# Optimization experiments

Hardware: AMD Instinct MI355X
Metric: run time of the kernel (lower is better)

The kernel has to match this reference:

```python
import jax, jax.numpy as jnp
import numpy as np
import math

QK_DIM = 128

def setup_inputs() -> dict:
    key = jax.random.key(0)
    kx, kq, kk, kv = jax.random.split(key, 4)
    B, S, D, H = 4, 4096, 1024, 128
    X = jax.random.normal(kx, (B, S, D), dtype=jnp.float32)
    # xavier-normal-ish scale for weights
    std = math.sqrt(2.0 / (D + H))
    W_q = jax.random.normal(kq, (D, H), dtype=jnp.float32) * std
    W_k = jax.random.normal(kk, (D, H), dtype=jnp.float32) * std
    W_v = jax.random.normal(kv, (D, H), dtype=jnp.float32) * std
    return {"X": X, "W_q": W_q, "W_k": W_k, "W_v": W_v}

def reference(X, W_q, W_k, W_v):
    # X: [B, S, D]; single-head causal attention
    Q = X @ W_q                       # [B, S, H]
    K = X @ W_k                       # [B, S, H]
    V = X @ W_v                       # [B, S, H]
    S_len = X.shape[1]
    scores = jnp.einsum('bsh,bth->bst', Q, K) / math.sqrt(QK_DIM)  # [B, S, S]
    causal = jnp.tril(jnp.ones((S_len, S_len), dtype=bool))
    scores = jnp.where(causal, scores, -jnp.inf)
    attn = jax.nn.softmax(scores, axis=-1)
    return jnp.einsum('bst,bth->bsh', attn, V)
```

## Files before the change

### kernel.cpp

```cpp
#include <hip/hip_runtime.h>
#include <hip/hip_bf16.h>

#define B_ 4
#define S_ 4096
#define D_ 1024
#define H_ 128

typedef unsigned short u16;
typedef unsigned int u32;
typedef short s16x8 __attribute__((ext_vector_type(8)));
typedef float f32x4 __attribute__((ext_vector_type(4)));
typedef float f32x16 __attribute__((ext_vector_type(16)));

__device__ __forceinline__ u16 f2bf(float f) {
    u32 x = __float_as_uint(f);
    u32 r = x + 0x7fffu + ((x >> 16) & 1u);
    return (u16)(r >> 16);
}

__device__ __forceinline__ u32 cvtpk_bf16(float a, float b) {
    u32 r;
    asm("v_cvt_pk_bf16_f32 %0, %1, %2" : "=v"(r) : "v"(a), "v"(b));
    return r;
}
__device__ __forceinline__ void pl32swap(u32& x, u32& y) {
    asm("v_permlane32_swap_b32 %0, %1" : "+v"(x), "+v"(y));
}

__device__ __forceinline__ void gl_lds16(const u16* g, u16* l) {
    __builtin_amdgcn_global_load_lds(
        (const __attribute__((address_space(1))) u32*)g,
        (__attribute__((address_space(3))) u32*)l, 16, 0, 0);
}

__global__ void detect_dtype_kernel(const u32* __restrict__ w, int* __restrict__ flag) {
    __shared__ int smax[256];
    const int tid = threadIdx.x;
    int m = 0;
    for (int i = tid; i < 1024; i += 256) {
        u32 x = w[i];
        m = max(m, max((int)((x >> 7) & 0xFF), (int)((x >> 23) & 0xFF)));
    }
    smax[tid] = m;
    __syncthreads();
    if (tid == 0) {
        int mm = 0;
        for (int i = 0; i < 256; ++i) mm = max(mm, smax[i]);
        *flag = (mm >= 200) ? 1 : 0;
    }
}

__global__ __launch_bounds__(256) void prep_w_kernel(
    const void* __restrict__ Wq, const void* __restrict__ Wk, const void* __restrict__ Wv,
    u16* __restrict__ Wt, const int* __restrict__ dflag)
{
    const int kt = blockIdx.x, mat = blockIdx.y;
    const void* W = (mat == 0) ? Wq : (mat == 1) ? Wk : Wv;
    const int isf = *dflag;
    const int t = threadIdx.x;
    const int kk = t >> 3;
    const int n0 = (t & 7) * 16;
    u16 vals[16];
    if (isf) {
        const float* wp = (const float*)W + (size_t)(kt * 32 + kk) * H_ + n0;
#pragma unroll
        for (int i = 0; i < 16; ++i) vals[i] = f2bf(wp[i]);
    } else {
        const u16* wp = (const u16*)W + (size_t)(kt * 32 + kk) * H_ + n0;
#pragma unroll
        for (int i = 0; i < 16; ++i) vals[i] = wp[i];
    }
    const size_t base = (size_t)(mat * 32 + kt) * 128;
#pragma unroll
    for (int i = 0; i < 16; ++i)
        Wt[(base + n0 + i) * 32 + kk] = vals[i];
}

__global__ __launch_bounds__(256) void qkv_kernel(
    const void* __restrict__ Xv, const u16* __restrict__ Wt,
    u16* __restrict__ Qo, u16* __restrict__ Ko, u16* __restrict__ Vto,
    const int* __restrict__ dflag)
{
    __shared__ u16 Ws[2][384 * 32];
    __shared__ union { u16 qk[32 * 136]; u16 vt[128 * 40]; } OsU;

    const int isf = *dflag;
    const int tid = threadIdx.x;
    const int w = tid >> 6, lane = tid & 63;
    const int r = lane & 15, q = lane >> 4;
    const size_t m0 = (size_t)blockIdx.x * 32;

    f32x4 acc[2][6];
#pragma unroll
    for (int s2 = 0; s2 < 2; ++s2)
#pragma unroll
        for (int i = 0; i < 6; ++i) acc[s2][i] = (f32x4){0.f, 0.f, 0.f, 0.f};

    const float* xf0 = (const float*)Xv + (m0 + r) * D_;
    const float* xf1 = (const float*)Xv + (m0 + 16 + r) * D_;
    const u16*   xb0 = (const u16*)Xv + (m0 + r) * D_;
    const u16*   xb1 = (const u16*)Xv + (m0 + 16 + r) * D_;

    float4 af[2][2];
    uint4  ab[2];

#pragma unroll
    for (int i = 0; i < 6; ++i) {
        int c = tid + i * 256;
        gl_lds16(Wt + (size_t)((c >> 9) * 32) * 4096 + (c & 511) * 8, &Ws[0][c * 8]);
    }
    if (isf) {
        af[0][0] = *(const float4*)(xf0 + q * 8);
        af[0][1] = *(const float4*)(xf0 + q * 8 + 4);
        af[1][0] = *(const float4*)(xf1 + q * 8);
        af[1][1] = *(const float4*)(xf1 + q * 8 + 4);
    } else {
        ab[0] = *(const uint4*)(xb0 + q * 8);
        ab[1] = *(const uint4*)(xb1 + q * 8);
    }

    for (int kt = 0; kt < 32; ++kt) {
        const int buf = kt & 1;
        __syncthreads();

        if (kt + 1 < 32) {
#pragma unroll
            for (int i = 0; i < 6; ++i) {
                int c = tid + i * 256;
                gl_lds16(Wt + (size_t)((c >> 9) * 32 + kt + 1) * 4096 + (c & 511) * 8,
                         &Ws[buf ^ 1][c * 8]);
            }
        }

        s16x8 a[2];
        if (isf) {
#pragma unroll
            for (int s2 = 0; s2 < 2; ++s2) {
                union { u16 u[8]; s16x8 v; } pk;
                pk.u[0] = f2bf(af[s2][0].x); pk.u[1] = f2bf(af[s2][0].y);
                pk.u[2] = f2bf(af[s2][0].z); pk.u[3] = f2bf(af[s2][0].w);
                pk.u[4] = f2bf(af[s2][1].x); pk.u[5] = f2bf(af[s2][1].y);
                pk.u[6] = f2bf(af[s2][1].z); pk.u[7] = f2bf(af[s2][1].w);
                a[s2] = pk.v;
            }
        } else {
            a[0] = *(const s16x8*)&ab[0];
            a[1] = *(const s16x8*)&ab[1];
        }

        if (kt + 1 < 32) {
            const int k0 = (kt + 1) * 32;
            if (isf) {
                af[0][0] = *(const float4*)(xf0 + k0 + q * 8);
                af[0][1] = *(const float4*)(xf0 + k0 + q * 8 + 4);
                af[1][0] = *(const float4*)(xf1 + k0 + q * 8);
                af[1][1] = *(const float4*)(xf1 + k0 + q * 8 + 4);
            } else {
                ab[0] = *(const uint4*)(xb0 + k0 + q * 8);
                ab[1] = *(const uint4*)(xb1 + k0 + q * 8);
            }
        }

#pragma unroll
        for (int i = 0; i < 6; ++i) {
            int c = w * 6 + i;
            s16x8 b = *(const s16x8*)&Ws[buf][(c >> 3) * 4096 + ((c & 7) * 16 + r) * 32 + q * 8];
            acc[0][i] = __builtin_amdgcn_mfma_f32_16x16x32_bf16(a[0], b, acc[0][i], 0, 0, 0);
            acc[1][i] = __builtin_amdgcn_mfma_f32_16x16x32_bf16(a[1], b, acc[1][i], 0, 0, 0);
        }
    }

    u16* outs[2] = {Qo, Ko};
    for (int m = 0; m < 2; ++m) {
        const float sc = (m == 0) ? 0.08838834764831845f : 1.0f;
        __syncthreads();
#pragma unroll
        for (int i = 0; i < 6; ++i) {
            int c = w * 6 + i;
            if ((c >> 3) == m) {
                int nt = c & 7;
#pragma unroll
                for (int s2 = 0; s2 < 2; ++s2)
#pragma unroll
                    for (int reg = 0; reg < 4; ++reg)
                        OsU.qk[(s2 * 16 + q * 4 + reg) * 136 + nt * 16 + r] = f2bf(acc[s2][i][reg] * sc);
            }
        }
        __syncthreads();
        u16* Out = outs[m];
#pragma unroll
        for (int it = 0; it < 2; ++it) {
            int c = tid + it * 256;
            int row = c >> 4, col = (c & 15) * 8;
            *(uint4*)(Out + (m0 + row) * H_ + col) = *(const uint4*)&OsU.qk[row * 136 + col];
        }
    }

    __syncthreads();
#pragma unroll
    for (int i = 0; i < 6; ++i) {
        int c = w * 6 + i;
        if ((c >> 3) == 2) {
            int nt = c & 7;
#pragma unroll
            for (int s2 = 0; s2 < 2; ++s2)
#pragma unroll
                for (int reg = 0; reg < 4; ++reg)
                    OsU.vt[(nt * 16 + r) * 40 + s2 * 16 + q * 4 + reg] = f2bf(acc[s2][i][reg]);
        }
    }
    __syncthreads();
    {
        const int bb = blockIdx.x >> 7;
        const int s0 = (blockIdx.x & 127) * 32;
#pragma unroll
        for (int it = 0; it < 2; ++it) {
            int c = tid + it * 256;
            int h = c >> 2, sh = (c & 3) * 8;
            *(uint4*)(Vto + ((size_t)bb * H_ + h) * S_ + s0 + sh) =
                *(const uint4*)&OsU.vt[h * 40 + sh];
        }
    }
}

__global__ __launch_bounds__(512) void attn_pair_kernel(
    const u16* __restrict__ Q, const u16* __restrict__ K, const u16* __restrict__ Vt,
    void* __restrict__ out, float* __restrict__ OP, float* __restrict__ LP,
    const int* __restrict__ dflag)
{
    __shared__ u16 Ks[2][128 * 128];
    __shared__ u16 Vs[2][128 * 128];
    __shared__ float lpS[8][32];

    const int isf = *dflag;
    const int tid = threadIdx.x;
    const int w = tid >> 6, lane = tid & 63;
    const int l31 = lane & 31, hi = lane >> 5;
    const int qs = w >> 2;
    const int kh = w & 3;
    const int bid = blockIdx.x;
    const int b = bid & 3;
    const int p = (bid >> 2) & 31;
    const int c = bid >> 7;
    const int nA = (p >> 1) + 1;
    const int m = 17 - nA;

    const u16* Kg  = K  + (size_t)b * S_ * H_;
    const u16* Vtg = Vt + (size_t)b * H_ * S_;

    for (int seg = 0; seg < 2; ++seg) {
        int qt, jlo, jhi;
        bool direct;
        if (seg == 0) {
            if (c != 0) continue;
            qt = p; jlo = 0; jhi = nA; direct = true;
        } else {
            qt = 63 - p;
            const int nB = ((63 - p) >> 1) + 1;
            jlo = (c == 0) ? 0 : m; jhi = (c == 0) ? m : nB; direct = false;
        }
        const int nT = (qt >> 1) + 1;
        const u16* Qg = Q + ((size_t)b * S_ + (size_t)qt * 64) * H_;

        s16x8 qf[8];
#pragma unroll
        for (int sl = 0; sl < 8; ++sl)
            qf[sl] = *(const s16x8*)(Qg + (size_t)(qs * 32 + l31) * H_ + sl * 16 + hi * 8);

        f32x16 accO[4];
#pragma unroll
        for (int hg = 0; hg < 4; ++hg)
#pragma unroll
            for (int i = 0; i < 16; ++i) accO[hg][i] = 0.f;
        float lp = 0.f;

        {
            const int j0 = jlo;
#pragma unroll
            for (int i = 0; i < 4; ++i) {
                int ck = tid + i * 512;
                int row = ck >> 4;
                int wo = ((ck & 15) * 16) ^ ((row & 7) << 4);
                gl_lds16(Kg + ((size_t)j0 * 128 + row) * H_ + (wo >> 1), &Ks[0][ck * 8]);
                gl_lds16(Vtg + (size_t)row * S_ + j0 * 128 + (wo >> 1), &Vs[0][ck * 8]);
            }
        }

        for (int j = jlo; j < jhi; ++j) {
            const int buf = (j - jlo) & 1;
            __syncthreads();

            if (j + 1 < jhi) {
                const int jn = j + 1;
#pragma unroll
                for (int i = 0; i < 4; ++i) {
                    int ck = tid + i * 512;
                    int row = ck >> 4;
                    int wo = ((ck & 15) * 16) ^ ((row & 7) << 4);
                    gl_lds16(Kg + ((size_t)jn * 128 + row) * H_ + (wo >> 1), &Ks[buf ^ 1][ck * 8]);
                    gl_lds16(Vtg + (size_t)row * S_ + jn * 128 + (wo >> 1), &Vs[buf ^ 1][ck * 8]);
                }
            }

            const int kr = kh * 32 + l31;
            const u16* kbase = &Ks[buf][kr * 128];
            s16x8 kf[8];
#pragma unroll
            for (int sl = 0; sl < 8; ++sl)
                kf[sl] = *(const s16x8*)&kbase[((sl * 32 + hi * 16) ^ ((kr & 7) << 4)) >> 1];

            f32x16 s0, s1;
#pragma unroll
            for (int i = 0; i < 16; ++i) { s0[i] = 0.f; s1[i] = 0.f; }
#pragma unroll
            for (int sl = 0; sl < 4; ++sl) {
                s0 = __builtin_amdgcn_mfma_f32_32x32x16_bf16(kf[sl], qf[sl], s0, 0, 0, 0);
                s1 = __builtin_amdgcn_mfma_f32_32x32x16_bf16(kf[sl + 4], qf[sl + 4], s1, 0, 0, 0);
            }

            s16x8 vf[4][2];
#pragma unroll
            for (int hg = 0; hg < 4; ++hg) {
                const int h = hg * 32 + l31;
                const u16* vbase = &Vs[buf][h * 128];
#pragma unroll
                for (int ks = 0; ks < 2; ++ks)
                    vf[hg][ks] = *(const s16x8*)&vbase[((kh * 64 + ks * 32 + hi * 16) ^ ((h & 7) << 4)) >> 1];
            }

            const bool diag = (j == nT - 1);
            float pv16[16];
#pragma unroll
            for (int r = 0; r < 16; ++r) {
                float s = fminf(s0[r] + s1[r], 80.f);
                float pv = __expf(s);
                int gkey = j * 128 + kh * 32 + ((r & 3) + 8 * (r >> 2) + 4 * hi);
                int grow = qt * 64 + qs * 32 + l31;
                if (diag && gkey > grow) pv = 0.f;
                lp += pv;
                pv16[r] = pv;
            }

            u32 w01 = cvtpk_bf16(pv16[0], pv16[1]),  w23 = cvtpk_bf16(pv16[2], pv16[3]);
            u32 w45 = cvtpk_bf16(pv16[4], pv16[5]),  w67 = cvtpk_bf16(pv16[6], pv16[7]);
            pl32swap(w01, w45);
            pl32swap(w23, w67);
            u32 x01 = cvtpk_bf16(pv16[8], pv16[9]),   x23 = cvtpk_bf16(pv16[10], pv16[11]);
            u32 x45 = cvtpk_bf16(pv16[12], pv16[13]), x67 = cvtpk_bf16(pv16[14], pv16[15]);
            pl32swap(x01, x45);
            pl32swap(x23, x67);
            union { u32 u[4]; s16x8 v; } pa0, pa1;
            pa0.u[0] = w01; pa0.u[1] = w23; pa0.u[2] = w45; pa0.u[3] = w67;
            pa1.u[0] = x01; pa1.u[1] = x23; pa1.u[2] = x45; pa1.u[3] = x67;

#pragma unroll
            for (int hg = 0; hg < 4; ++hg) {
                accO[hg] = __builtin_amdgcn_mfma_f32_32x32x16_bf16(pa0.v, vf[hg][0], accO[hg], 0, 0, 0);
                accO[hg] = __builtin_amdgcn_mfma_f32_32x32x16_bf16(pa1.v, vf[hg][1], accO[hg], 0, 0, 0);
            }
        }

        lp += __shfl_xor(lp, 32);
        if (lane < 32) lpS[w][l31] = lp;
        __syncthreads();

        float* opSf = (float*)&Ks[0][0];
        for (int s = 0; s < 4; ++s) {
            if (kh == s) {
                float* dst = opSf + qs * 32 * 128;
#pragma unroll
                for (int hg = 0; hg < 4; ++hg)
#pragma unroll
                    for (int r = 0; r < 16; ++r) {
                        int idx = ((r & 3) + 8 * (r >> 2) + 4 * hi) * 128 + hg * 32 + l31;
                        if (s == 0) dst[idx] = accO[hg][r];
                        else        dst[idx] += accO[hg][r];
                    }
            }
            __syncthreads();
        }

        const int row = tid >> 3;
        const int col = (tid & 7) * 16;
        const int rq = row & 31, rs = row >> 5;
        const float lrow = lpS[rs * 4 + 0][rq] + lpS[rs * 4 + 1][rq] +
                           lpS[rs * 4 + 2][rq] + lpS[rs * 4 + 3][rq];
        const float* src = opSf + (rs * 32 + rq) * 128 + col;

        if (direct) {
            const float inv = 1.0f / lrow;
            const size_t orow = (size_t)b * S_ + (size_t)qt * 64 + row;
            if (isf) {
                float* dst = (float*)out + orow * H_ + col;
#pragma unroll
                for (int i = 0; i < 4; ++i) {
                    float4 v = *(const float4*)(src + i * 4);
                    v.x *= inv; v.y *= inv; v.z *= inv; v.w *= inv;
                    *(float4*)(dst + i * 4) = v;
                }
            } else {
                u16* dst = (u16*)out + orow * H_ + col;
#pragma unroll
                for (int hh = 0; hh < 2; ++hh) {
                    union { u16 u[8]; uint4 v; } pk;
#pragma unroll
                    for (int i = 0; i < 8; ++i) pk.u[i] = f2bf(src[hh * 8 + i] * inv);
                    *(uint4*)(dst + hh * 8) = pk.v;
                }
            }
        } else {
            const size_t slot = (size_t)((b * 32 + p) * 2 + c);
            float* Os = OP + slot * 64 * 128;
#pragma unroll
            for (int i = 0; i < 4; ++i)
                *(float4*)(Os + row * 128 + col + i * 4) = *(const float4*)(src + i * 4);
            if (tid < 64)
                LP[slot * 64 + tid] = lpS[(tid >> 5) * 4 + 0][tid & 31] + lpS[(tid >> 5) * 4 + 1][tid & 31] +
                                      lpS[(tid >> 5) * 4 + 2][tid & 31] + lpS[(tid >> 5) * 4 + 3][tid & 31];
        }
        __syncthreads();
    }
}

__global__ __launch_bounds__(256) void combine_kernel(
    const float* __restrict__ OP, const float* __restrict__ LP,
    void* __restrict__ out, const int* __restrict__ dflag)
{
    const int isf = *dflag;
    const int bid = blockIdx.x;
    const int b = bid >> 5;
    const int qtl = bid & 31;
    const int p = 31 - qtl;
    const size_t s0 = (size_t)((b * 32 + p) * 2);
    const int tid = threadIdx.x;
    const int row = tid >> 2;
    const int col0 = (tid & 3) * 32;

    const float* O0 = OP + (s0 * 64 + row) * 128 + col0;
    const float* O1 = OP + ((s0 + 1) * 64 + row) * 128 + col0;
    const float l = LP[s0 * 64 + row] + LP[(s0 + 1) * 64 + row];
    const float inv = 1.0f / l;

    float vals[32];
#pragma unroll
    for (int i = 0; i < 8; ++i) {
        float4 a = *(const float4*)(O0 + i * 4);
        float4 bb = *(const float4*)(O1 + i * 4);
        vals[i * 4 + 0] = (a.x + bb.x) * inv;
        vals[i * 4 + 1] = (a.y + bb.y) * inv;
        vals[i * 4 + 2] = (a.z + bb.z) * inv;
        vals[i * 4 + 3] = (a.w + bb.w) * inv;
    }

    const size_t orow = (size_t)b * S_ + (size_t)(32 + qtl) * 64 + row;
    if (isf) {
        float* dst = (float*)out + orow * H_ + col0;
#pragma unroll
        for (int i = 0; i < 8; ++i)
            *(float4*)(dst + i * 4) = *(const float4*)(&vals[i * 4]);
    } else {
        u16* dst = (u16*)out + orow * H_ + col0;
#pragma unroll
        for (int hh = 0; hh < 4; ++hh) {
            union { u16 u[8]; uint4 v; } pk;
#pragma unroll
            for (int i = 0; i < 8; ++i) pk.u[i] = f2bf(vals[hh * 8 + i]);
            *(uint4*)(dst + hh * 8) = pk.v;
        }
    }
}

extern "C" void kernel_launch(void* const* d_in, const int* in_sizes, int n_in,
                              void* d_out, int out_size, void* d_ws, size_t ws_size,
                              hipStream_t stream) {
    (void)in_sizes; (void)n_in; (void)out_size; (void)ws_size;
    const void* X  = d_in[0];
    const void* Wq = d_in[1];
    const void* Wk = d_in[2];
    const void* Wv = d_in[3];

    int* dflag = (int*)d_ws;
    u16* Qw = (u16*)((char*)d_ws + 256);
    const size_t n = (size_t)B_ * S_ * H_;
    u16* Kw = Qw + n;
    u16* Vtw = Kw + n;
    u16* Wt = Vtw + n;
    float* OP = (float*)(Wt + 3 * 1024 * 128);
    float* LP = OP + (size_t)256 * 64 * 128;

    detect_dtype_kernel<<<1, 256, 0, stream>>>((const u32*)Wq, dflag);
    prep_w_kernel<<<dim3(32, 3), 256, 0, stream>>>(Wq, Wk, Wv, Wt, dflag);
    qkv_kernel<<<512, 256, 0, stream>>>(X, Wt, Qw, Kw, Vtw, dflag);
    attn_pair_kernel<<<256, 512, 0, stream>>>(Qw, Kw, Vtw, d_out, OP, LP, dflag);
    combine_kernel<<<128, 256, 0, stream>>>(OP, LP, d_out, dflag);
}
```

Before: 191.9 us.

## Double M-tile in QKV projection and stage X through swizzled LDS

The QKV projection kernel now processes 64 rows per block with 512 threads, so each staged weight tile is reused by two row-groups of waves and total weight traffic from L2 is halved. X tiles are loaded asynchronously into double-buffered, XOR-swizzled LDS instead of through per-lane register prefetch. The output staging buffers are aliased onto the weight buffer. This trades fewer blocks (256 instead of 512) and more LDS reads for better weight reuse and an overlapped X load.

```diff
diff --git a/kernel.cpp b/kernel.cpp
--- a/kernel.cpp
+++ b/kernel.cpp
@@ -76,19 +76,23 @@
         Wt[(base + n0 + i) * 32 + kk] = vals[i];
 }
 
-__global__ __launch_bounds__(256) void qkv_kernel(
+__global__ __launch_bounds__(512) void qkv_kernel(
     const void* __restrict__ Xv, const u16* __restrict__ Wt,
     u16* __restrict__ Qo, u16* __restrict__ Ko, u16* __restrict__ Vto,
     const int* __restrict__ dflag)
 {
     __shared__ u16 Ws[2][384 * 32];
-    __shared__ union { u16 qk[32 * 136]; u16 vt[128 * 40]; } OsU;
+    __shared__ float Asf[2][64 * 32];
 
     const int isf = *dflag;
     const int tid = threadIdx.x;
     const int w = tid >> 6, lane = tid & 63;
+    const int ws = w >> 2, wc = w & 3;
     const int r = lane & 15, q = lane >> 4;
-    const size_t m0 = (size_t)blockIdx.x * 32;
+    const size_t m0 = (size_t)blockIdx.x * 64;
+
+    const float* Xf = (const float*)Xv;
+    const u16*   Xb = (const u16*)Xv;
 
     f32x4 acc[2][6];
 #pragma unroll
@@ -96,27 +100,19 @@
 #pragma unroll
         for (int i = 0; i < 6; ++i) acc[s2][i] = (f32x4){0.f, 0.f, 0.f, 0.f};
 
-    const float* xf0 = (const float*)Xv + (m0 + r) * D_;
-    const float* xf1 = (const float*)Xv + (m0 + 16 + r) * D_;
-    const u16*   xb0 = (const u16*)Xv + (m0 + r) * D_;
-    const u16*   xb1 = (const u16*)Xv + (m0 + 16 + r) * D_;
-
-    float4 af[2][2];
-    uint4  ab[2];
-
-#pragma unroll
-    for (int i = 0; i < 6; ++i) {
-        int c = tid + i * 256;
+#pragma unroll
+    for (int i = 0; i < 3; ++i) {
+        int c = tid + i * 512;
         gl_lds16(Wt + (size_t)((c >> 9) * 32) * 4096 + (c & 511) * 8, &Ws[0][c * 8]);
     }
     if (isf) {
-        af[0][0] = *(const float4*)(xf0 + q * 8);
-        af[0][1] = *(const float4*)(xf0 + q * 8 + 4);
-        af[1][0] = *(const float4*)(xf1 + q * 8);
-        af[1][1] = *(const float4*)(xf1 + q * 8 + 4);
-    } else {
-        ab[0] = *(const uint4*)(xb0 + q * 8);
-        ab[1] = *(const uint4*)(xb1 + q * 8);
+        int ck = tid;
+        int row = ck >> 3, co = (ck & 7) ^ (row & 7);
+        gl_lds16((const u16*)(Xf + (m0 + row) * D_ + co * 4), (u16*)&Asf[0][ck * 4]);
+    } else if (tid < 256) {
+        int ck = tid;
+        int row = ck >> 2, co = (ck & 3) ^ (row & 3);
+        gl_lds16(Xb + (m0 + row) * D_ + co * 8, (u16*)&Asf[0][0] + ck * 8);
     }
 
     for (int kt = 0; kt < 32; ++kt) {
@@ -125,45 +121,53 @@
 
         if (kt + 1 < 32) {
 #pragma unroll
-            for (int i = 0; i < 6; ++i) {
-                int c = tid + i * 256;
+            for (int i = 0; i < 3; ++i) {
+                int c = tid + i * 512;
                 gl_lds16(Wt + (size_t)((c >> 9) * 32 + kt + 1) * 4096 + (c & 511) * 8,
                          &Ws[buf ^ 1][c * 8]);
             }
+            const int k0 = (kt + 1) * 32;
+            if (isf) {
+                int ck = tid;
+                int row = ck >> 3, co = (ck & 7) ^ (row & 7);
+                gl_lds16((const u16*)(Xf + (m0 + row) * D_ + k0 + co * 4),
+                         (u16*)&Asf[buf ^ 1][ck * 4]);
+            } else if (tid < 256) {
+                int ck = tid;
+                int row = ck >> 2, co = (ck & 3) ^ (row & 3);
+                gl_lds16(Xb + (m0 + row) * D_ + k0 + co * 8,
+                         (u16*)&Asf[buf ^ 1][0] + ck * 8);
+            }
         }
 
         s16x8 a[2];
         if (isf) {
 #pragma unroll
             for (int s2 = 0; s2 < 2; ++s2) {
+                const int row = ws * 32 + s2 * 16 + r;
+                const int sw = row & 7;
+                const float* ap = &Asf[buf][row * 32];
+                float4 fa = *(const float4*)&ap[((2 * q) ^ sw) * 4];
+                float4 fb = *(const float4*)&ap[((2 * q + 1) ^ sw) * 4];
                 union { u16 u[8]; s16x8 v; } pk;
-                pk.u[0] = f2bf(af[s2][0].x); pk.u[1] = f2bf(af[s2][0].y);
-                pk.u[2] = f2bf(af[s2][0].z); pk.u[3] = f2bf(af[s2][0].w);
-                pk.u[4] = f2bf(af[s2][1].x); pk.u[5] = f2bf(af[s2][1].y);
-                pk.u[6] = f2bf(af[s2][1].z); pk.u[7] = f2bf(af[s2][1].w);
+                pk.u[0] = f2bf(fa.x); pk.u[1] = f2bf(fa.y);
+                pk.u[2] = f2bf(fa.z); pk.u[3] = f2bf(fa.w);
+                pk.u[4] = f2bf(fb.x); pk.u[5] = f2bf(fb.y);
+                pk.u[6] = f2bf(fb.z); pk.u[7] = f2bf(fb.w);
                 a[s2] = pk.v;
             }
         } else {
-            a[0] = *(const s16x8*)&ab[0];
-            a[1] = *(const s16x8*)&ab[1];
-        }
-
-        if (kt + 1 < 32) {
-            const int k0 = (kt + 1) * 32;
-            if (isf) {
-                af[0][0] = *(const float4*)(xf0 + k0 + q * 8);
-                af[0][1] = *(const float4*)(xf0 + k0 + q * 8 + 4);
-                af[1][0] = *(const float4*)(xf1 + k0 + q * 8);
-                af[1][1] = *(const float4*)(xf1 + k0 + q * 8 + 4);
-            } else {
-                ab[0] = *(const uint4*)(xb0 + k0 + q * 8);
-                ab[1] = *(const uint4*)(xb1 + k0 + q * 8);
+            const u16* ab = (const u16*)&Asf[buf][0];
+#pragma unroll
+            for (int s2 = 0; s2 < 2; ++s2) {
+                const int row = ws * 32 + s2 * 16 + r;
+                a[s2] = *(const s16x8*)&ab[row * 32 + ((q ^ (row & 3)) * 8)];
             }
         }
 
 #pragma unroll
         for (int i = 0; i < 6; ++i) {
-            int c = w * 6 + i;
+            int c = wc * 6 + i;
             s16x8 b = *(const s16x8*)&Ws[buf][(c >> 3) * 4096 + ((c & 7) * 16 + r) * 32 + q * 8];
             acc[0][i] = __builtin_amdgcn_mfma_f32_16x16x32_bf16(a[0], b, acc[0][i], 0, 0, 0);
             acc[1][i] = __builtin_amdgcn_mfma_f32_16x16x32_bf16(a[1], b, acc[1][i], 0, 0, 0);
@@ -171,54 +175,58 @@
     }
 
     u16* outs[2] = {Qo, Ko};
+    u16* qk = &Ws[0][0];
     for (int m = 0; m < 2; ++m) {
         const float sc = (m == 0) ? 0.08838834764831845f : 1.0f;
         __syncthreads();
 #pragma unroll
         for (int i = 0; i < 6; ++i) {
-            int c = w * 6 + i;
+            int c = wc * 6 + i;
             if ((c >> 3) == m) {
                 int nt = c & 7;
 #pragma unroll
                 for (int s2 = 0; s2 < 2; ++s2)
 #pragma unroll
                     for (int reg = 0; reg < 4; ++reg)
-                        OsU.qk[(s2 * 16 + q * 4 + reg) * 136 + nt * 16 + r] = f2bf(acc[s2][i][reg] * sc);
+                        qk[(ws * 32 + s2 * 16 + q * 4 + reg) * 136 + nt * 16 + r] =
+                            f2bf(acc[s2][i][reg] * sc);
             }
         }
         __syncthreads();
         u16* Out = outs[m];
 #pragma unroll
         for (int it = 0; it < 2; ++it) {
-            int c = tid + it * 256;
-            int row = c >> 4, col = (c & 15) * 8;
-            *(uint4*)(Out + (m0 + row) * H_ + col) = *(const uint4*)&OsU.qk[row * 136 + col];
+            int c2 = tid + it * 512;
+            int row = c2 >> 4, col = (c2 & 15) * 8;
+            *(uint4*)(Out + (m0 + row) * H_ + col) = *(const uint4*)&qk[row * 136 + col];
         }
     }
 
     __syncthreads();
+    u16* vt = &Ws[0][0];
 #pragma unroll
     for (int i = 0; i < 6; ++i) {
-        int c = w * 6 + i;
+        int c = wc * 6 + i;
         if ((c >> 3) == 2) {
             int nt = c & 7;
 #pragma unroll
             for (int s2 = 0; s2 < 2; ++s2)
 #pragma unroll
                 for (int reg = 0; reg < 4; ++reg)
-                    OsU.vt[(nt * 16 + r) * 40 + s2 * 16 + q * 4 + reg] = f2bf(acc[s2][i][reg]);
+                    vt[(nt * 16 + r) * 72 + ws * 32 + s2 * 16 + q * 4 + reg] =
+                        f2bf(acc[s2][i][reg]);
         }
     }
     __syncthreads();
     {
-        const int bb = blockIdx.x >> 7;
-        const int s0 = (blockIdx.x & 127) * 32;
+        const int bb = blockIdx.x >> 6;
+        const int s0 = (blockIdx.x & 63) * 64;
 #pragma unroll
         for (int it = 0; it < 2; ++it) {
-            int c = tid + it * 256;
-            int h = c >> 2, sh = (c & 3) * 8;
+            int c2 = tid + it * 512;
+            int h = c2 >> 3, sh = (c2 & 7) * 8;
             *(uint4*)(Vto + ((size_t)bb * H_ + h) * S_ + s0 + sh) =
-                *(const uint4*)&OsU.vt[h * 40 + sh];
+                *(const uint4*)&vt[h * 72 + sh];
         }
     }
 }
@@ -490,7 +498,7 @@
 
     detect_dtype_kernel<<<1, 256, 0, stream>>>((const u32*)Wq, dflag);
     prep_w_kernel<<<dim3(32, 3), 256, 0, stream>>>(Wq, Wk, Wv, Wt, dflag);
-    qkv_kernel<<<512, 256, 0, stream>>>(X, Wt, Qw, Kw, Vtw, dflag);
+    qkv_kernel<<<256, 512, 0, stream>>>(X, Wt, Qw, Kw, Vtw, dflag);
     attn_pair_kernel<<<256, 512, 0, stream>>>(Qw, Kw, Vtw, d_out, OP, LP, dflag);
     combine_kernel<<<128, 256, 0, stream>>>(OP, LP, d_out, dflag);
 }
```

After: 184.5 us. 1.04x faster.
